# Optimization experiments

Hardware: AMD Instinct MI355X
Metric: run time of the kernel (lower is better)

Reference implementation:

```python
import jax, jax.numpy as jnp
import numpy as np

B, N, D = 4, 4096, 256

def setup_inputs() -> dict:
    key = jax.random.key(0)
    ks = jax.random.split(key, 7)
    def xavier(k, shape):
        fan_in, fan_out = shape[1], shape[0]
        a = jnp.sqrt(6.0 / (fan_in + fan_out))
        return jax.random.uniform(k, shape, jnp.float32, -a, a)
    return {
        "x": jax.random.normal(ks[0], (B, N, D), jnp.float32),
        "Wq": xavier(ks[1], (D, D)),
        "bq": jnp.zeros((D,), jnp.float32),
        "Wk": xavier(ks[2], (D, D)),
        "bk": jnp.zeros((D,), jnp.float32),
        "Wv": xavier(ks[3], (D, D)),
        "bv": jnp.zeros((D,), jnp.float32),
        "scale": jnp.asarray([jnp.sqrt(jnp.float32(D))]),
    }

def reference(x, Wq, bq, Wk, bk, Wv, bv, scale):
    # nn.Linear: y = x @ W.T + b
    q = jnp.einsum('bnd,ed->bne', x, Wq) + bq
    k = jnp.einsum('bnd,ed->bne', x, Wk) + bk
    v = jnp.einsum('bnd,ed->bne', x, Wv) + bv
    scores = jnp.einsum('bqd,bkd->bqk', q, k) / scale[0]  # [B,N,N]
    attn = jax.nn.softmax(scores, axis=-1)
    out = jnp.einsum('bqk,bkd->bqd', attn, v)
    return out
```

## Files before the change

### kernel.cpp

```cpp
#include <hip/hip_runtime.h>
#include <hip/hip_bf16.h>

typedef unsigned int u32;
typedef unsigned short u16;
typedef __attribute__((ext_vector_type(8))) __bf16 bf8v;
typedef __attribute__((ext_vector_type(16))) float f32x16;
typedef __attribute__((ext_vector_type(8))) u16 u16x8;

__device__ inline u16 f2bf(float f) {
    u32 u = __float_as_uint(f);
    u = (u + 0x7FFF + ((u >> 16) & 1)) >> 16;
    return (u16)u;
}
__device__ inline u32 pk2(float a, float b) {
    return (u32)f2bf(a) | ((u32)f2bf(b) << 16);
}
__device__ inline float bf2f(u16 h) { return __uint_as_float(((u32)h) << 16); }

__device__ inline void dma16(const u16* g, u16* l) {
    __builtin_amdgcn_global_load_lds(
        (const __attribute__((address_space(1))) void*)g,
        (__attribute__((address_space(3))) void*)l, 16, 0, 0);
}

__global__ void cvt_all(const float* __restrict__ x,
                        const float* __restrict__ wq, const float* __restrict__ wk,
                        const float* __restrict__ wv,
                        u16* __restrict__ xp, u16* __restrict__ wall) {
    const int blk = blockIdx.x;
    if (blk < 2048) {
        int g = blk * 256 + threadIdx.x;
        int row = g >> 5, cp = g & 31;
        const float* s = x + row * 256 + cp * 8;
        float4 a = *(const float4*)s;
        float4 b = *(const float4*)(s + 4);
        uint4 o;
        o.x = pk2(a.x, a.y); o.y = pk2(a.z, a.w);
        o.z = pk2(b.x, b.y); o.w = pk2(b.z, b.w);
        *(uint4*)(xp + (row >> 5) * 8192 + cp * 256 + (row & 31) * 8) = o;
    } else {
        const int bb = blk - 2048;
        const int m = bb >> 5;
        const float* src = m == 0 ? wq : m == 1 ? wk : wv;
        int g = (bb & 31) * 256 + threadIdx.x;
        int row = g >> 5, c = g & 31;
        const float* s = src + row * 256 + c * 8;
        float4 a = *(const float4*)s;
        float4 b = *(const float4*)(s + 4);
        uint4 o;
        o.x = pk2(a.x, a.y); o.y = pk2(a.z, a.w);
        o.z = pk2(b.x, b.y); o.w = pk2(b.z, b.w);
        *(uint4*)(wall + m * 65536 + row * 256 + ((c ^ (row & 7)) * 8)) = o;
    }
}

__global__ __launch_bounds__(256) void qkv_proj(
    const u16* __restrict__ xp, const u16* __restrict__ wall,
    const float* __restrict__ bq, const float* __restrict__ bk, const float* __restrict__ bv,
    u16* __restrict__ qp, u16* __restrict__ kp, u16* __restrict__ vp)
{
    __shared__ u16 Ws[64 * 256];

    const int blk = blockIdx.x;
    const int xcd = blk & 7;
    const int s2 = blk >> 3;
    const int rt = s2 / 12;
    const int yz = s2 % 12;
    const int sel = yz >> 2;
    const int colbase = (yz & 3) * 64;
    const int rowbase0 = (xcd * 16 + rt) * 128;

    const float* bias = sel == 0 ? bq : sel == 1 ? bk : bv;
    const int tid = threadIdx.x;
    const int wave = tid >> 6, lane = tid & 63;
    const int l31 = lane & 31, l5 = lane >> 5;
    const int tg = (rowbase0 >> 5) + wave;

    {
        const u16* wsrc = wall + sel * 65536 + colbase * 256;
#pragma unroll
        for (int j = 0; j < 8; j++) {
            const int i = wave * 8 + j;
            dma16(wsrc + i * 512 + lane * 8, Ws + i * 512);
        }
    }
    asm volatile("s_waitcnt vmcnt(0)" ::: "memory");
    __syncthreads();

    f32x16 acc0, acc1;
#pragma unroll
    for (int j = 0; j < 16; j++) { acc0[j] = 0.f; acc1[j] = 0.f; }

    const u16* ap = xp + tg * 8192 + l5 * 256 + l31 * 8;
    const int sw = l31 & 7;
#pragma unroll
    for (int kk = 0; kk < 16; kk++) {
        bf8v af = *(const bf8v*)(ap + kk * 512);
        bf8v b0 = *(const bf8v*)(Ws + l31 * 256 + (((kk * 2 + l5) ^ sw) * 8));
        bf8v b1 = *(const bf8v*)(Ws + (32 + l31) * 256 + (((kk * 2 + l5) ^ sw) * 8));
        acc0 = __builtin_amdgcn_mfma_f32_32x32x16_bf16(af, b0, acc0, 0, 0, 0);
        acc1 = __builtin_amdgcn_mfma_f32_32x32x16_bf16(af, b1, acc1, 0, 0, 0);
    }

    const float bias0 = bias[colbase + l31], bias1 = bias[colbase + 32 + l31];
    if (sel < 2) {
        u16* base = (sel == 0 ? qp : kp) + tg * 8192;
        const int c0 = (colbase >> 3) + (l31 >> 3), j0 = l31 & 7;
#pragma unroll
        for (int r = 0; r < 16; r++) {
            const int R = (r & 3) + 8 * (r >> 2) + 4 * l5;
            base[c0 * 256 + R * 8 + j0]       = f2bf(acc0[r] + bias0);
            base[(c0 + 4) * 256 + R * 8 + j0] = f2bf(acc1[r] + bias1);
        }
    } else {
        u16* base = vp + tg * 8192;
        const int d0 = colbase + l31, d1 = d0 + 32;
#pragma unroll
        for (int r = 0; r < 16; r++) {
            const int R = (r & 3) + 8 * (r >> 2) + 4 * l5;
            base[(R >> 3) * 2048 + d0 * 8 + (R & 7)] = f2bf(acc0[r] + bias0);
            base[(R >> 3) * 2048 + d1 * 8 + (R & 7)] = f2bf(acc1[r] + bias1);
        }
    }
}

__global__ __launch_bounds__(256, 2) void flash_attn(
    const u16* __restrict__ qp_, const u16* __restrict__ kp_, const u16* __restrict__ vp_,
    const float* __restrict__ scale,
    u16* __restrict__ Opb, float* __restrict__ ml)
{
    __shared__ u16 Ks[2 * 8192];
    __shared__ u16 Vs[2 * 8192];
    __shared__ u16 Ps[4 * 1152];

    const int tid = threadIdx.x;
    const int wave = tid >> 6, lane = tid & 63;
    const int l31 = lane & 31, l5 = lane >> 5;

    const int blk = blockIdx.x;
    const int slot = blk >> 3;
    const int g = (blk & 7) * 2 + (slot >> 5);
    const int qtile = slot & 31;
    const int b = g >> 2, s = g & 3;
    const int qbase = qtile * 128 + wave * 32;
    const float is2 = 1.44269504088896f / scale[0];

    union { u16x8 u; bf8v v; } oneu;
#pragma unroll
    for (int j = 0; j < 8; j++) oneu.u[j] = 0x3F80;
    const bf8v ones = oneu.v;

    bf8v qf[16];
    {
        const u16* qp = qp_ + (b * 128 + qtile * 4 + wave) * 8192 + l31 * 8;
#pragma unroll
        for (int kk = 0; kk < 16; kk++)
            qf[kk] = *(const bf8v*)(qp + (kk * 2 + l5) * 256);
    }

    f32x16 o[8];
#pragma unroll
    for (int i = 0; i < 8; i++)
#pragma unroll
        for (int j = 0; j < 16; j++) o[i][j] = 0.f;
    f32x16 ls;
#pragma unroll
    for (int j = 0; j < 16; j++) ls[j] = 0.f;

    const u16* kbase = kp_ + (b * 128 + s * 32) * 8192;
    const u16* vbase = vp_ + (b * 128 + s * 32) * 8192;
    u16* pw = Ps + wave * 1152;

#pragma unroll
    for (int j = 0; j < 4; j++) {
        const int i = wave * 4 + j;
        dma16(kbase + i * 512 + lane * 8, Ks + i * 512);
    }
#pragma unroll
    for (int j = 0; j < 4; j++) {
        const int i = wave * 4 + j;
        dma16(vbase + i * 512 + lane * 8, Vs + i * 512);
    }
#pragma unroll
    for (int j = 0; j < 4; j++) {
        const int i = wave * 4 + j;
        dma16(kbase + 8192 + i * 512 + lane * 8, Ks + 8192 + i * 512);
    }
    asm volatile("s_waitcnt vmcnt(8)" ::: "memory");
    asm volatile("s_barrier" ::: "memory");

    bf8v pf0, pf1;
    {
        f32x16 c0, c1;
#pragma unroll
        for (int j = 0; j < 16; j++) { c0[j] = 0.f; c1[j] = 0.f; }
#pragma unroll
        for (int j = 0; j < 8; j++) {
            bf8v kf0 = *(const bf8v*)(Ks + (j * 2 + l5) * 256 + l31 * 8);
            c0 = __builtin_amdgcn_mfma_f32_32x32x16_bf16(qf[j], kf0, c0, 0, 0, 0);
            bf8v kf1 = *(const bf8v*)(Ks + ((8 + j) * 2 + l5) * 256 + l31 * 8);
            c1 = __builtin_amdgcn_mfma_f32_32x32x16_bf16(qf[8 + j], kf1, c1, 0, 0, 0);
        }
#pragma unroll
        for (int r = 0; r < 16; r++) {
            const int R = (r & 3) + 8 * (r >> 2) + 4 * l5;
            pw[R * 36 + l31] = f2bf(exp2f((c0[r] + c1[r]) * is2));
        }
        asm volatile("s_waitcnt lgkmcnt(0)" ::: "memory");
        pf0 = *(const bf8v*)(pw + l31 * 36 + l5 * 8);
        pf1 = *(const bf8v*)(pw + l31 * 36 + 16 + l5 * 8);
    }

#pragma unroll 1
    for (int it = 0; it < 31; it++) {
        const int buf = it & 1;
        asm volatile("s_waitcnt vmcnt(0)" ::: "memory");
        asm volatile("s_barrier" ::: "memory");

        const u16* Kb_ = Ks + (buf ^ 1) * 8192;
        const u16* Vb_ = Vs + buf * 8192;

        __builtin_amdgcn_s_setprio(1);
        f32x16 c0, c1;
#pragma unroll
        for (int j = 0; j < 16; j++) { c0[j] = 0.f; c1[j] = 0.f; }
        ls = __builtin_amdgcn_mfma_f32_32x32x16_bf16(pf0, ones, ls, 0, 0, 0);
        ls = __builtin_amdgcn_mfma_f32_32x32x16_bf16(pf1, ones, ls, 0, 0, 0);

        {
            const u16* vt_ = vbase + (it + 1) * 8192;
#pragma unroll
            for (int j = 0; j < 4; j++) {
                const int i = wave * 4 + j;
                dma16(vt_ + i * 512 + lane * 8, Vs + (buf ^ 1) * 8192 + i * 512);
            }
            if (it < 30) {
                const u16* kt_ = kbase + (it + 2) * 8192;
#pragma unroll
                for (int j = 0; j < 4; j++) {
                    const int i = wave * 4 + j;
                    dma16(kt_ + i * 512 + lane * 8, Ks + buf * 8192 + i * 512);
                }
            }
        }

#pragma unroll
        for (int j = 0; j < 8; j++) {
            bf8v kf0 = *(const bf8v*)(Kb_ + (j * 2 + l5) * 256 + l31 * 8);
            c0 = __builtin_amdgcn_mfma_f32_32x32x16_bf16(qf[j], kf0, c0, 0, 0, 0);
            bf8v vf0 = *(const bf8v*)(Vb_ + (l5 * 256 + j * 32 + l31) * 8);
            o[j] = __builtin_amdgcn_mfma_f32_32x32x16_bf16(pf0, vf0, o[j], 0, 0, 0);
            bf8v kf1 = *(const bf8v*)(Kb_ + ((8 + j) * 2 + l5) * 256 + l31 * 8);
            c1 = __builtin_amdgcn_mfma_f32_32x32x16_bf16(qf[8 + j], kf1, c1, 0, 0, 0);
            bf8v vf1 = *(const bf8v*)(Vb_ + ((2 + l5) * 256 + j * 32 + l31) * 8);
            o[j] = __builtin_amdgcn_mfma_f32_32x32x16_bf16(pf1, vf1, o[j], 0, 0, 0);
        }
        __builtin_amdgcn_s_setprio(0);

#pragma unroll
        for (int r = 0; r < 16; r++) {
            const int R = (r & 3) + 8 * (r >> 2) + 4 * l5;
            pw[R * 36 + l31] = f2bf(exp2f((c0[r] + c1[r]) * is2));
        }
        asm volatile("s_waitcnt lgkmcnt(0)" ::: "memory");
        pf0 = *(const bf8v*)(pw + l31 * 36 + l5 * 8);
        pf1 = *(const bf8v*)(pw + l31 * 36 + 16 + l5 * 8);
    }

    asm volatile("s_waitcnt vmcnt(0)" ::: "memory");
    asm volatile("s_barrier" ::: "memory");
    {
        const u16* Vb_ = Vs + 8192;
        __builtin_amdgcn_s_setprio(1);
        ls = __builtin_amdgcn_mfma_f32_32x32x16_bf16(pf0, ones, ls, 0, 0, 0);
        ls = __builtin_amdgcn_mfma_f32_32x32x16_bf16(pf1, ones, ls, 0, 0, 0);
#pragma unroll
        for (int j = 0; j < 8; j++) {
            bf8v vf0 = *(const bf8v*)(Vb_ + (l5 * 256 + j * 32 + l31) * 8);
            o[j] = __builtin_amdgcn_mfma_f32_32x32x16_bf16(pf0, vf0, o[j], 0, 0, 0);
            bf8v vf1 = *(const bf8v*)(Vb_ + ((2 + l5) * 256 + j * 32 + l31) * 8);
            o[j] = __builtin_amdgcn_mfma_f32_32x32x16_bf16(pf1, vf1, o[j], 0, 0, 0);
        }
        __builtin_amdgcn_s_setprio(0);
    }

    const int rowg = s * 16384 + b * 4096 + qbase;
    u16* ob = Opb + (size_t)rowg * 256;
#pragma unroll
    for (int nb = 0; nb < 8; nb++)
#pragma unroll
        for (int r = 0; r < 16; r++) {
            const int R = (r & 3) + 8 * (r >> 2) + 4 * l5;
            ob[R * 256 + nb * 32 + l31] = f2bf(o[nb][r]);
        }
    if (l31 == 0)
#pragma unroll
        for (int r = 0; r < 16; r++) {
            const int R = (r & 3) + 8 * (r >> 2) + 4 * l5;
            ml[rowg + R] = ls[r];
        }
}

__global__ __launch_bounds__(256) void combine(
    const u16* __restrict__ Opb, const float* __restrict__ ml, float* __restrict__ out)
{
    const int row = blockIdx.x * 4 + (threadIdx.x >> 6);
    const int lane = threadIdx.x & 63;
    const float denom = ml[row] + ml[16384 + row] + ml[32768 + row] + ml[49152 + row];
    float4 acc = {0.f, 0.f, 0.f, 0.f};
#pragma unroll
    for (int si = 0; si < 4; si++) {
        ushort4 v = *(const ushort4*)(Opb + ((size_t)si * 16384 + row) * 256 + lane * 4);
        acc.x += bf2f(v.x); acc.y += bf2f(v.y);
        acc.z += bf2f(v.z); acc.w += bf2f(v.w);
    }
    const float inv = 1.0f / denom;
    acc.x *= inv; acc.y *= inv; acc.z *= inv; acc.w *= inv;
    *((float4*)(out + (size_t)row * 256) + lane) = acc;
}

extern "C" void kernel_launch(void* const* d_in, const int* in_sizes, int n_in,
                              void* d_out, int out_size, void* d_ws, size_t ws_size,
                              hipStream_t stream) {
    const float* x     = (const float*)d_in[0];
    const float* Wq    = (const float*)d_in[1];
    const float* bq    = (const float*)d_in[2];
    const float* Wk    = (const float*)d_in[3];
    const float* bk    = (const float*)d_in[4];
    const float* Wv    = (const float*)d_in[5];
    const float* bv    = (const float*)d_in[6];
    const float* scale = (const float*)d_in[7];
    float* out = (float*)d_out;

    char* ws = (char*)d_ws;
    u16* xp   = (u16*)ws;
    u16* qp   = (u16*)(ws + (8u  << 20));
    u16* kp   = (u16*)(ws + (16u << 20));
    u16* vp   = (u16*)(ws + (24u << 20));
    u16* wall = (u16*)(ws + (32u << 20));
    u16* Opb  = (u16*)(ws + (34u << 20));
    float* ml = (float*)(ws + (66u << 20));

    cvt_all<<<2144, 256, 0, stream>>>(x, Wq, Wk, Wv, xp, wall);
    qkv_proj<<<1536, 256, 0, stream>>>(xp, wall, bq, bk, bv, qp, kp, vp);
    flash_attn<<<512, 256, 0, stream>>>(qp, kp, vp, scale, Opb, ml);
    combine<<<4096, 256, 0, stream>>>(Opb, ml, out);
}
```

Before: 202.9 us.

## Keep softmax probabilities in registers via transposed QK MFMA and permlane swap

Swaps the MFMA operands for QK^T so the score tile comes out transposed, then builds the P operand for the PV MFMA directly in registers using packed bf16 conversion and v_permlane32_swap. This removes the per-wave LDS round trip for P (stores, lgkmcnt wait, reloads) and the Ps shared buffer. It also moves the exp2 work in between the PV MFMAs so it can overlap with matrix work, uses the hardware exp2 builtin, and drops the s_setprio hints. The risk is that the lane mapping is subtly wrong, and the interleaving increases register pressure.

After: 182.8 us. 1.11x faster.

```diff
diff --git a/kernel.cpp b/kernel.cpp
--- a/kernel.cpp
+++ b/kernel.cpp
@@ -16,6 +16,15 @@
     return (u32)f2bf(a) | ((u32)f2bf(b) << 16);
 }
 __device__ inline float bf2f(u16 h) { return __uint_as_float(((u32)h) << 16); }
+
+__device__ inline u32 cvtpk(float a, float b) {
+    u32 r;
+    asm("v_cvt_pk_bf16_f32 %0, %1, %2" : "=v"(r) : "v"(a), "v"(b));
+    return r;
+}
+__device__ inline void plswap(u32& a, u32& b) {
+    asm("v_permlane32_swap_b32 %0, %1" : "+v"(a), "+v"(b));
+}
 
 __device__ inline void dma16(const u16* g, u16* l) {
     __builtin_amdgcn_global_load_lds(
@@ -131,7 +140,6 @@
 {
     __shared__ u16 Ks[2 * 8192];
     __shared__ u16 Vs[2 * 8192];
-    __shared__ u16 Ps[4 * 1152];
 
     const int tid = threadIdx.x;
     const int wave = tid >> 6, lane = tid & 63;
@@ -169,7 +177,6 @@
 
     const u16* kbase = kp_ + (b * 128 + s * 32) * 8192;
     const u16* vbase = vp_ + (b * 128 + s * 32) * 8192;
-    u16* pw = Ps + wave * 1152;
 
 #pragma unroll
     for (int j = 0; j < 4; j++) {
@@ -197,18 +204,24 @@
 #pragma unroll
         for (int j = 0; j < 8; j++) {
             bf8v kf0 = *(const bf8v*)(Ks + (j * 2 + l5) * 256 + l31 * 8);
-            c0 = __builtin_amdgcn_mfma_f32_32x32x16_bf16(qf[j], kf0, c0, 0, 0, 0);
+            c0 = __builtin_amdgcn_mfma_f32_32x32x16_bf16(kf0, qf[j], c0, 0, 0, 0);
             bf8v kf1 = *(const bf8v*)(Ks + ((8 + j) * 2 + l5) * 256 + l31 * 8);
-            c1 = __builtin_amdgcn_mfma_f32_32x32x16_bf16(qf[8 + j], kf1, c1, 0, 0, 0);
-        }
-#pragma unroll
-        for (int r = 0; r < 16; r++) {
-            const int R = (r & 3) + 8 * (r >> 2) + 4 * l5;
-            pw[R * 36 + l31] = f2bf(exp2f((c0[r] + c1[r]) * is2));
-        }
-        asm volatile("s_waitcnt lgkmcnt(0)" ::: "memory");
-        pf0 = *(const bf8v*)(pw + l31 * 36 + l5 * 8);
-        pf1 = *(const bf8v*)(pw + l31 * 36 + 16 + l5 * 8);
+            c1 = __builtin_amdgcn_mfma_f32_32x32x16_bf16(kf1, qf[8 + j], c1, 0, 0, 0);
+        }
+        float e[16];
+#pragma unroll
+        for (int r = 0; r < 16; r++)
+            e[r] = __builtin_amdgcn_exp2f((c0[r] + c1[r]) * is2);
+        u32 pA = cvtpk(e[0], e[1]), pB = cvtpk(e[2], e[3]);
+        u32 pC = cvtpk(e[4], e[5]), pD = cvtpk(e[6], e[7]);
+        plswap(pA, pC); plswap(pB, pD);
+        u32 pE = cvtpk(e[8], e[9]),  pF = cvtpk(e[10], e[11]);
+        u32 pG = cvtpk(e[12], e[13]), pH = cvtpk(e[14], e[15]);
+        plswap(pE, pG); plswap(pF, pH);
+        union { uint4 u; bf8v v; } u0, u1;
+        u0.u = (uint4){pA, pB, pC, pD};
+        u1.u = (uint4){pE, pF, pG, pH};
+        pf0 = u0.v; pf1 = u1.v;
     }
 
 #pragma unroll 1
@@ -216,17 +229,6 @@
         const int buf = it & 1;
         asm volatile("s_waitcnt vmcnt(0)" ::: "memory");
         asm volatile("s_barrier" ::: "memory");
-
-        const u16* Kb_ = Ks + (buf ^ 1) * 8192;
-        const u16* Vb_ = Vs + buf * 8192;
-
-        __builtin_amdgcn_s_setprio(1);
-        f32x16 c0, c1;
-#pragma unroll
-        for (int j = 0; j < 16; j++) { c0[j] = 0.f; c1[j] = 0.f; }
-        ls = __builtin_amdgcn_mfma_f32_32x32x16_bf16(pf0, ones, ls, 0, 0, 0);
-        ls = __builtin_amdgcn_mfma_f32_32x32x16_bf16(pf1, ones, ls, 0, 0, 0);
-
         {
             const u16* vt_ = vbase + (it + 1) * 8192;
 #pragma unroll
@@ -243,35 +245,48 @@
                 }
             }
         }
-
+        const u16* Kb_ = Ks + (buf ^ 1) * 8192;
+        f32x16 c0, c1;
+#pragma unroll
+        for (int j = 0; j < 16; j++) { c0[j] = 0.f; c1[j] = 0.f; }
 #pragma unroll
         for (int j = 0; j < 8; j++) {
             bf8v kf0 = *(const bf8v*)(Kb_ + (j * 2 + l5) * 256 + l31 * 8);
-            c0 = __builtin_amdgcn_mfma_f32_32x32x16_bf16(qf[j], kf0, c0, 0, 0, 0);
+            c0 = __builtin_amdgcn_mfma_f32_32x32x16_bf16(kf0, qf[j], c0, 0, 0, 0);
+            bf8v kf1 = *(const bf8v*)(Kb_ + ((8 + j) * 2 + l5) * 256 + l31 * 8);
+            c1 = __builtin_amdgcn_mfma_f32_32x32x16_bf16(kf1, qf[8 + j], c1, 0, 0, 0);
+        }
+        const u16* Vb_ = Vs + buf * 8192;
+        ls = __builtin_amdgcn_mfma_f32_32x32x16_bf16(pf0, ones, ls, 0, 0, 0);
+        ls = __builtin_amdgcn_mfma_f32_32x32x16_bf16(pf1, ones, ls, 0, 0, 0);
+        float e[16];
+#pragma unroll
+        for (int j = 0; j < 8; j++) {
             bf8v vf0 = *(const bf8v*)(Vb_ + (l5 * 256 + j * 32 + l31) * 8);
             o[j] = __builtin_amdgcn_mfma_f32_32x32x16_bf16(pf0, vf0, o[j], 0, 0, 0);
-            bf8v kf1 = *(const bf8v*)(Kb_ + ((8 + j) * 2 + l5) * 256 + l31 * 8);
-            c1 = __builtin_amdgcn_mfma_f32_32x32x16_bf16(qf[8 + j], kf1, c1, 0, 0, 0);
+            e[2 * j] = __builtin_amdgcn_exp2f((c0[2 * j] + c1[2 * j]) * is2);
             bf8v vf1 = *(const bf8v*)(Vb_ + ((2 + l5) * 256 + j * 32 + l31) * 8);
             o[j] = __builtin_amdgcn_mfma_f32_32x32x16_bf16(pf1, vf1, o[j], 0, 0, 0);
-        }
-        __builtin_amdgcn_s_setprio(0);
-
-#pragma unroll
-        for (int r = 0; r < 16; r++) {
-            const int R = (r & 3) + 8 * (r >> 2) + 4 * l5;
-            pw[R * 36 + l31] = f2bf(exp2f((c0[r] + c1[r]) * is2));
-        }
-        asm volatile("s_waitcnt lgkmcnt(0)" ::: "memory");
-        pf0 = *(const bf8v*)(pw + l31 * 36 + l5 * 8);
-        pf1 = *(const bf8v*)(pw + l31 * 36 + 16 + l5 * 8);
+            e[2 * j + 1] = __builtin_amdgcn_exp2f((c0[2 * j + 1] + c1[2 * j + 1]) * is2);
+        }
+        {
+            u32 pA = cvtpk(e[0], e[1]), pB = cvtpk(e[2], e[3]);
+            u32 pC = cvtpk(e[4], e[5]), pD = cvtpk(e[6], e[7]);
+            plswap(pA, pC); plswap(pB, pD);
+            u32 pE = cvtpk(e[8], e[9]),  pF = cvtpk(e[10], e[11]);
+            u32 pG = cvtpk(e[12], e[13]), pH = cvtpk(e[14], e[15]);
+            plswap(pE, pG); plswap(pF, pH);
+            union { uint4 u; bf8v v; } u0, u1;
+            u0.u = (uint4){pA, pB, pC, pD};
+            u1.u = (uint4){pE, pF, pG, pH};
+            pf0 = u0.v; pf1 = u1.v;
+        }
     }
 
     asm volatile("s_waitcnt vmcnt(0)" ::: "memory");
     asm volatile("s_barrier" ::: "memory");
     {
         const u16* Vb_ = Vs + 8192;
-        __builtin_amdgcn_s_setprio(1);
         ls = __builtin_amdgcn_mfma_f32_32x32x16_bf16(pf0, ones, ls, 0, 0, 0);
         ls = __builtin_amdgcn_mfma_f32_32x32x16_bf16(pf1, ones, ls, 0, 0, 0);
 #pragma unroll
@@ -281,7 +296,6 @@
             bf8v vf1 = *(const bf8v*)(Vb_ + ((2 + l5) * 256 + j * 32 + l31) * 8);
             o[j] = __builtin_amdgcn_mfma_f32_32x32x16_bf16(pf1, vf1, o[j], 0, 0, 0);
         }
-        __builtin_amdgcn_s_setprio(0);
     }
 
     const int rowg = s * 16384 + b * 4096 + qbase;
```
